# Kernel optimization log

Hardware: AMD Instinct MI355X
Metric: run time of the kernel (lower is better)

The kernel has to match this reference:

```python
import jax, jax.numpy as jnp
import numpy as np

B, NPG, EPG = 8, 12500, 200000
N, E = B * NPG, B * EPG
NUM_CLASSES = 10
EPS = 1e-5
G1, G2 = 8, 4            # voxel grids: size 1/8 then 1/4 over unit square
C1 = B * G1 * G1         # coarse node count after pool5
DIMS = [(1, 16), (16, 64), (64, 64), (64, 64), (64, 128), (128, 128), (128, 128)]


def _bn_elu(x, g, b):
    # training-mode BatchNorm1d (biased var) + ELU
    m = jnp.mean(x, axis=0)
    v = jnp.var(x, axis=0)
    return jax.nn.elu(g * (x - m) * jax.lax.rsqrt(v + EPS) + b)


def _pnconv(x, pos, src, dst, wl, wg, n):
    # PointNetConv: gather endpoints, local_nn on [x_j, pos_j - pos_i], scatter-max, global_nn
    h = jnp.concatenate([x[src], pos[src] - pos[dst]], axis=-1) @ wl
    agg = jax.ops.segment_max(h, dst, num_segments=n)
    agg = jnp.where(jnp.isfinite(agg), agg, 0.0)
    return agg @ wg


def _voxel_cluster(pos2d, batch, g, cells):
    cx = jnp.clip(jnp.floor(pos2d[:, 0] * g), 0, g - 1).astype(jnp.int32)
    cy = jnp.clip(jnp.floor(pos2d[:, 1] * g), 0, g - 1).astype(jnp.int32)
    return batch.astype(jnp.int32) * cells + cx * g + cy


def _forward(x, pos, src, dst, batch, params):
    (wl1, wg1, g1, b1, wl2, wg2, g2, b2, wl3, wg3, g3, b3,
     wl4, wg4, g4, b4, wl5, wg5, g5, b5, wl6, wg6, g6, b6,
     wl7, wg7, g7, b7, wfc) = params
    h = _bn_elu(_pnconv(x, pos, src, dst, wl1, wg1, N), g1, b1)
    h = _bn_elu(_pnconv(h, pos, src, dst, wl2, wg2, N), g2, b2)
    sc = h
    h = _bn_elu(_pnconv(h, pos, src, dst, wl3, wg3, N), g3, b3)
    h = _bn_elu(_pnconv(h, pos, src, dst, wl4, wg4, N), g4, b4)
    h = h + sc
    h = _bn_elu(_pnconv(h, pos, src, dst, wl5, wg5, N), g5, b5)
    # pool5: voxel max-pool of x, mean-pool of pos, coarsen edges
    clus = _voxel_cluster(pos[:, :2], batch, G1, G1 * G1)
    hc = jax.ops.segment_max(h, clus, num_segments=C1)
    hc = jnp.where(jnp.isfinite(hc), hc, 0.0)
    cnt = jax.ops.segment_sum(jnp.ones((N,), h.dtype), clus, num_segments=C1)
    posc = jax.ops.segment_sum(pos, clus, num_segments=C1) / jnp.maximum(cnt, 1.0)[:, None]
    loops = jnp.arange(C1)
    src2 = jnp.concatenate([clus[src], loops])
    dst2 = jnp.concatenate([clus[dst], loops])
    batchc = jnp.repeat(jnp.arange(B), G1 * G1)
    sc2 = hc
    h2 = _bn_elu(_pnconv(hc, posc, src2, dst2, wl6, wg6, C1), g6, b6)
    h2 = _bn_elu(_pnconv(h2, posc, src2, dst2, wl7, wg7, C1), g7, b7)
    h2 = h2 + sc2
    # pool7: 4x4 voxel max-pool -> fixed 16 cells per graph
    clus2 = _voxel_cluster(posc[:, :2], batchc, G2, G2 * G2)
    xo = jax.ops.segment_max(h2, clus2, num_segments=B * 16)
    xo = jnp.where(jnp.isfinite(xo), xo, 0.0)
    return xo.reshape(B, 16 * 128) @ wfc


def setup_inputs() -> dict:
    key = jax.random.key(0)
    ks = jax.random.split(key, 24)
    x = jax.random.normal(ks[0], (N, 1), jnp.float32)
    pos = jax.random.uniform(ks[1], (N, 3), jnp.float32)
    off = (jnp.arange(B) * NPG)[:, None]
    src = (jax.random.randint(ks[2], (B, EPG), 0, NPG) + off).reshape(-1)
    dst = (jax.random.randint(ks[3], (B, EPG), 0, NPG) + off).reshape(-1)
    loops = jnp.arange(N)
    src = jnp.concatenate([src, loops])
    dst = jnp.concatenate([dst, loops])
    batch = jnp.repeat(jnp.arange(B), NPG)
    inp = dict(x=x, pos=pos, src=src, dst=dst, batch=batch)
    ki = 4
    for i, (cin, cout) in enumerate(DIMS, 1):
        inp[f"wl{i}"] = jax.random.normal(ks[ki], (cin + 3, cout), jnp.float32) * (1.0 / np.sqrt(cin + 3))
        ki += 1
        inp[f"wg{i}"] = jax.random.normal(ks[ki], (cout, cout), jnp.float32) * (1.0 / np.sqrt(cout))
        ki += 1
        inp[f"g{i}"] = jnp.ones((cout,), jnp.float32)
        inp[f"b{i}"] = jnp.zeros((cout,), jnp.float32)
    inp["wfc"] = jax.random.normal(ks[ki], (128 * 16, NUM_CLASSES), jnp.float32) * (1.0 / np.sqrt(2048.0))
    return inp


def reference(x, pos, src, dst, batch,
              wl1, wg1, g1, b1, wl2, wg2, g2, b2, wl3, wg3, g3, b3,
              wl4, wg4, g4, b4, wl5, wg5, g5, b5, wl6, wg6, g6, b6,
              wl7, wg7, g7, b7, wfc):
    params = (wl1, wg1, g1, b1, wl2, wg2, g2, b2, wl3, wg3, g3, b3,
              wl4, wg4, g4, b4, wl5, wg5, g5, b5, wl6, wg6, g6, b6,
              wl7, wg7, g7, b7, wfc)
    return _forward(x, pos, src, dst, batch, params)
```

## Files before the change

kernel.cpp:

```cpp
#include <hip/hip_runtime.h>
#include <math.h>

#define N_NODES 100000
#define NPG     12500
#define EPG     200000
#define EPG_TOT 212500
#define E_TOT   1700000
#define C1      512
#define NB_SCAN 98
#define NSTRIPE 64
#define NCHUNK  8
#define CHUNK   26563

static inline int cdiv(int a, int b){ return (a + b - 1) / b; }

__device__ __forceinline__ unsigned fenc(float f){
  unsigned u = __float_as_uint(f);
  return (u >> 31) ? ~u : (u | 0x80000000u);
}
__device__ __forceinline__ float fdec(unsigned e){
  return (e & 0x80000000u) ? __uint_as_float(e ^ 0x80000000u) : __uint_as_float(~e);
}

__device__ __forceinline__ float elu1(float v){ return v > 0.f ? v : expm1f(v); }

__global__ void zero_kernel(int* __restrict__ p, int n){
  int i = blockIdx.x * 256 + threadIdx.x;
  if (i < n) p[i] = 0;
}

__global__ __launch_bounds__(1024) void count_deg(
    const int* __restrict__ dst, int* __restrict__ deg,
    unsigned short* __restrict__ ernk){
  __shared__ int ldeg[NPG];
  __shared__ int lbase[NPG];
  int g = blockIdx.x & 7;
  int chunk = blockIdx.x >> 3;
  int t = threadIdx.x;
  for (int j = t; j < NPG; j += 1024) ldeg[j] = 0;
  __syncthreads();
  int i0 = chunk * CHUNK;
  int i1 = min(i0 + CHUNK, EPG_TOT);
  for (int idx = i0 + t; idx < i1; idx += 1024){
    int dl = (idx < EPG) ? (dst[g * EPG + idx] - g * NPG) : (idx - EPG);
    int p = atomicAdd(&ldeg[dl], 1);
    ernk[(size_t)g * EPG_TOT + idx] = (unsigned short)p;
  }
  __syncthreads();
  for (int j = t; j < NPG; j += 1024){
    int cnt = ldeg[j];
    lbase[j] = cnt ? atomicAdd(&deg[g * NPG + j], cnt) : 0;
  }
  __syncthreads();
  for (int idx = i0 + t; idx < i1; idx += 1024){
    int dl = (idx < EPG) ? (dst[g * EPG + idx] - g * NPG) : (idx - EPG);
    ernk[(size_t)g * EPG_TOT + idx] += (unsigned short)lbase[dl];
  }
}

__global__ void scan1(const int* __restrict__ deg, int* __restrict__ row_start,
                      int* __restrict__ partials){
  __shared__ int sm[256];
  int t = threadIdx.x, b = blockIdx.x;
  int base = b * 1024 + t * 4;
  int d0 = (base + 0 < N_NODES) ? deg[base + 0] : 0;
  int d1 = (base + 1 < N_NODES) ? deg[base + 1] : 0;
  int d2 = (base + 2 < N_NODES) ? deg[base + 2] : 0;
  int d3 = (base + 3 < N_NODES) ? deg[base + 3] : 0;
  int s = d0 + d1 + d2 + d3;
  sm[t] = s; __syncthreads();
  for (int off = 1; off < 256; off <<= 1){
    int v = (t >= off) ? sm[t - off] : 0;
    __syncthreads();
    sm[t] += v;
    __syncthreads();
  }
  int excl = sm[t] - s;
  if (base + 0 < N_NODES) row_start[base + 0] = excl;
  if (base + 1 < N_NODES) row_start[base + 1] = excl + d0;
  if (base + 2 < N_NODES) row_start[base + 2] = excl + d0 + d1;
  if (base + 3 < N_NODES) row_start[base + 3] = excl + d0 + d1 + d2;
  if (t == 255) partials[b] = sm[255];
}

__global__ void scan2(int* __restrict__ partials){
  if (threadIdx.x == 0 && blockIdx.x == 0){
    int acc = 0;
    for (int i = 0; i < NB_SCAN; i++){ int v = partials[i]; partials[i] = acc; acc += v; }
  }
}

__global__ void scan3(int* __restrict__ row_start, const int* __restrict__ partials){
  int i = blockIdx.x * 256 + threadIdx.x;
  if (i < N_NODES) row_start[i] += partials[i >> 10];
  if (i == 0) row_start[N_NODES] = E_TOT;
}

__global__ void fill_csr(const int* __restrict__ src, const int* __restrict__ dst,
                         const int* __restrict__ clus, const unsigned short* __restrict__ ernk,
                         const int* __restrict__ row_start,
                         unsigned short* __restrict__ col, int* __restrict__ pf){
  int g = blockIdx.x & 7;
  int idx = (blockIdx.x >> 3) * 256 + threadIdx.x;
  if (idx >= EPG_TOT) return;
  int s, d;
  if (idx < EPG){ int e = g * EPG + idx; s = src[e]; d = dst[e]; }
  else { s = d = g * NPG + idx - EPG; }
  int p = ernk[(size_t)g * EPG_TOT + idx];
  col[row_start[d] + p] = (unsigned short)(s - g * NPG);
  pf[clus[d] * 64 + (clus[s] & 63)] = 1;
}

template<int R, int CIN, int COUT, bool FIX, bool STATS, bool BNIN, bool POSW, bool GSWZ>
__global__ __launch_bounds__(256) void gemm_tile(
    const float* __restrict__ in, const float* __restrict__ w,
    const float* __restrict__ ss, const float* __restrict__ resid,
    float* __restrict__ side, const float* __restrict__ posn,
    const float* __restrict__ w3p, float* __restrict__ out,
    float* __restrict__ stat, int n){
  constexpr int CPL = (COUT + 63) / 64;
  __shared__ float lds[4][R * CIN];
  __shared__ float sred[STATS ? 8 * COUT : 1];
  int wave = threadIdx.x >> 6, lane = threadIdx.x & 63;
  int base, nlim;
  if (GSWZ){
    int g = blockIdx.x & 7;
    base = g * NPG + ((blockIdx.x >> 3) * 4 + wave) * R;
    nlim = g * NPG + NPG;
  } else {
    base = (blockIdx.x * 4 + wave) * R;
    nlim = n;
  }

  if (base < nlim){
    const float4* src4 = (const float4*)(in + (size_t)base * CIN);
    const float4* res4 = resid ? (const float4*)(resid + (size_t)base * CIN) : nullptr;
    float4* side4 = side ? (float4*)(side + (size_t)base * CIN) : nullptr;
    float4* dst4 = (float4*)lds[wave];
    int n4 = min(R, nlim - base) * CIN / 4;
    for (int i = lane; i < R * CIN / 4; i += 64){
      float4 v = (i < n4) ? src4[i] : make_float4(0.f, 0.f, 0.f, 0.f);
      if (FIX){
        v.x = isfinite(v.x) ? v.x : 0.f; v.y = isfinite(v.y) ? v.y : 0.f;
        v.z = isfinite(v.z) ? v.z : 0.f; v.w = isfinite(v.w) ? v.w : 0.f;
      }
      if (BNIN){
        int c0 = (i * 4) & (CIN - 1);
        v.x = elu1(fmaf(v.x, ss[c0 + 0], ss[128 + c0 + 0]));
        v.y = elu1(fmaf(v.y, ss[c0 + 1], ss[128 + c0 + 1]));
        v.z = elu1(fmaf(v.z, ss[c0 + 2], ss[128 + c0 + 2]));
        v.w = elu1(fmaf(v.w, ss[c0 + 3], ss[128 + c0 + 3]));
        if (res4 && i < n4){
          float4 r = res4[i];
          v.x += r.x; v.y += r.y; v.z += r.z; v.w += r.w;
        }
        if (side4 && i < n4) side4[i] = v;
      }
      dst4[i] = v;
    }
  }
  __builtin_amdgcn_wave_barrier();

  bool act = (COUT >= 64) || (lane < COUT);
  float acc[CPL][R];
  #pragma unroll
  for (int j = 0; j < CPL; j++)
    #pragma unroll
    for (int r = 0; r < R; r++) acc[j][r] = 0.f;

  if (base < nlim && act){
    const float4* l4 = (const float4*)lds[wave];
    for (int k = 0; k < CIN; k += 4){
      float4 wv[CPL];
      #pragma unroll
      for (int j = 0; j < CPL; j++){
        int c = lane + 64 * j;
        wv[j].x = w[(k + 0) * COUT + c];
        wv[j].y = w[(k + 1) * COUT + c];
        wv[j].z = w[(k + 2) * COUT + c];
        wv[j].w = w[(k + 3) * COUT + c];
      }
      #pragma unroll
      for (int r = 0; r < R; r++){
        float4 a = l4[(r * CIN + k) >> 2];
        #pragma unroll
        for (int j = 0; j < CPL; j++)
          acc[j][r] = fmaf(a.x, wv[j].x, fmaf(a.y, wv[j].y,
                      fmaf(a.z, wv[j].z, fmaf(a.w, wv[j].w, acc[j][r]))));
      }
    }
    float q0[POSW ? CPL : 1], q1[POSW ? CPL : 1], q2[POSW ? CPL : 1];
    if (POSW){
      #pragma unroll
      for (int j = 0; j < CPL; j++){
        int c = lane + 64 * j;
        q0[j] = w3p[c]; q1[j] = w3p[COUT + c]; q2[j] = w3p[2 * COUT + c];
      }
    }
    int nrows = min(R, nlim - base);
    for (int r = 0; r < nrows; r++){
      if (POSW){
        float px = posn[(size_t)(base + r) * 3 + 0];
        float py = posn[(size_t)(base + r) * 3 + 1];
        float pz = posn[(size_t)(base + r) * 3 + 2];
        #pragma unroll
        for (int j = 0; j < CPL; j++)
          acc[j][r] = fmaf(px, q0[j], fmaf(py, q1[j], fmaf(pz, q2[j], acc[j][r])));
      }
      #pragma unroll
      for (int j = 0; j < CPL; j++)
        out[(size_t)(base + r) * COUT + lane + 64 * j] = acc[j][r];
    }
  }

  if (STATS){
    #pragma unroll
    for (int j = 0; j < CPL; j++){
      float s = 0.f, q = 0.f;
      #pragma unroll
      for (int r = 0; r < R; r++){ s += acc[j][r]; q += acc[j][r] * acc[j][r]; }
      if (act){
        int c = lane + 64 * j;
        sred[(2 * wave + 0) * COUT + c] = s;
        sred[(2 * wave + 1) * COUT + c] = q;
      }
    }
    __syncthreads();
    int c = threadIdx.x;
    if (c < COUT){
      float S = 0.f, Q = 0.f;
      #pragma unroll
      for (int wv = 0; wv < 4; wv++){
        S += sred[(2 * wv + 0) * COUT + c];
        Q += sred[(2 * wv + 1) * COUT + c];
      }
      float* st = stat + (size_t)(blockIdx.x & (NSTRIPE - 1)) * 256;
      atomicAdd(&st[c], S);
      atomicAdd(&st[128 + c], Q);
    }
  }
}

__global__ void node1_kernel(const float* __restrict__ x, const float* __restrict__ pos,
                             const float* __restrict__ wl, float* __restrict__ u){
  int i = blockIdx.x * 256 + threadIdx.x;
  if (i >= N_NODES * 16) return;
  int node = i >> 4, c = i & 15;
  float px = pos[node * 3 + 0], py = pos[node * 3 + 1], pz = pos[node * 3 + 2];
  u[i] = fmaf(x[node], wl[c],
         fmaf(px, wl[16 + c], fmaf(py, wl[32 + c], pz * wl[48 + c])));
}

template<int CPL>
__global__ __launch_bounds__(256) void edge_aggN(
    const float* __restrict__ u, int ushift,
    const unsigned short* __restrict__ col,
    const float* __restrict__ w3, int cout,
    const int* __restrict__ row_start, const float* __restrict__ pos,
    float* __restrict__ agg){
  int wave = threadIdx.x >> 6, lane = threadIdx.x & 63;
  int g = blockIdx.x & 7;
  int d = g * NPG + (blockIdx.x >> 3) * 4 + wave;
  const float* uu = u + ((size_t)(g * NPG) << ushift) + lane;
  int e0 = row_start[d], e1 = row_start[d + 1];
  float a0[CPL], a1[CPL], a2[CPL], a3[CPL];
  #pragma unroll
  for (int p = 0; p < CPL; p++){ a0[p] = a1[p] = a2[p] = a3[p] = -INFINITY; }
  for (int eb = e0; eb < e1; eb += 64){
    int m = min(64, e1 - eb);
    int sv = ((int)col[eb + min(lane, m - 1)]) << ushift;
    for (int j = 0; j < m; j += 4){
      int j1 = min(j + 1, m - 1), j2 = min(j + 2, m - 1), j3 = min(j + 3, m - 1);
      int s0 = __builtin_amdgcn_readlane(sv, j);
      int s1 = __builtin_amdgcn_readlane(sv, j1);
      int s2 = __builtin_amdgcn_readlane(sv, j2);
      int s3 = __builtin_amdgcn_readlane(sv, j3);
      #pragma unroll
      for (int p = 0; p < CPL; p++){
        a0[p] = fmaxf(a0[p], uu[s0 + 64 * p]);
        a1[p] = fmaxf(a1[p], uu[s1 + 64 * p]);
        a2[p] = fmaxf(a2[p], uu[s2 + 64 * p]);
        a3[p] = fmaxf(a3[p], uu[s3 + 64 * p]);
      }
    }
  }
  float px = pos[d * 3 + 0], py = pos[d * 3 + 1], pz = pos[d * 3 + 2];
  #pragma unroll
  for (int p = 0; p < CPL; p++){
    int c = lane + 64 * p;
    float w0 = w3[c], w1 = w3[cout + c], w2 = w3[2 * cout + c];
    float corr = fmaf(px, w0, fmaf(py, w1, pz * w2));
    agg[(size_t)d * cout + c] = fmaxf(fmaxf(a0[p], a1[p]), fmaxf(a2[p], a3[p])) - corr;
  }
}

__global__ __launch_bounds__(256) void edge_agg16(
    const float* __restrict__ u,
    const unsigned short* __restrict__ col,
    const float* __restrict__ w3,
    const int* __restrict__ row_start, const float* __restrict__ pos,
    float* __restrict__ agg){
  int wave = threadIdx.x >> 6, lane = threadIdx.x & 63;
  int slot = lane >> 4, c = lane & 15;
  int g = blockIdx.x & 7;
  int dloc = (blockIdx.x >> 3) * 16 + wave * 4 + slot;
  int d = g * NPG + dloc;
  bool vd = dloc < NPG;
  int e0 = vd ? row_start[d] : 0;
  int e1 = vd ? row_start[d + 1] : 0;
  int len = e1 - e0;
  int maxlen = max(len, __shfl_xor(len, 16, 64));
  maxlen = max(maxlen, __shfl_xor(maxlen, 32, 64));
  int cap = max(len - 1, 0);
  const float* uu = u + ((size_t)(g * NPG) << 4) + c;
  float acc0 = -INFINITY, acc1 = -INFINITY;
  for (int k = 0; k < maxlen; k += 2){
    int s0 = ((int)col[e0 + min(k, cap)]) << 4;
    int s1 = ((int)col[e0 + min(k + 1, cap)]) << 4;
    float h0 = uu[s0];
    float h1 = uu[s1];
    acc0 = (k < len) ? fmaxf(acc0, h0) : acc0;
    acc1 = (k + 1 < len) ? fmaxf(acc1, h1) : acc1;
  }
  if (vd){
    float w0 = w3[c], w1 = w3[16 + c], w2 = w3[32 + c];
    float px = pos[d * 3 + 0], py = pos[d * 3 + 1], pz = pos[d * 3 + 2];
    float corr = fmaf(px, w0, fmaf(py, w1, pz * w2));
    agg[d * 16 + c] = fmaxf(acc0, acc1) - corr;
  }
}

__global__ void bn_finalize(const float* __restrict__ stats, const float* __restrict__ g,
                            const float* __restrict__ b, int cout, float invn,
                            float* __restrict__ ss){
  int c = blockIdx.x;
  if (c >= cout) return;
  int l = threadIdx.x;
  float S = stats[l * 256 + c];
  float Q = stats[l * 256 + 128 + c];
  for (int off = 32; off > 0; off >>= 1){
    S += __shfl_down(S, off, 64);
    Q += __shfl_down(Q, off, 64);
  }
  if (l == 0){
    float mean = S * invn;
    float var = fmaxf(Q * invn - mean * mean, 0.f);
    float sc = g[c] * rsqrtf(var + 1e-5f);
    ss[c] = sc;
    ss[128 + c] = b[c] - mean * sc;
  }
}

__global__ void pool5_a(const float* __restrict__ pos, const int* __restrict__ batch,
                        int* __restrict__ clus, int* __restrict__ ccnt,
                        float* __restrict__ psum){
  int i = blockIdx.x * 256 + threadIdx.x;
  if (i >= N_NODES) return;
  int cx = min(max((int)floorf(pos[i * 3 + 0] * 8.f), 0), 7);
  int cy = min(max((int)floorf(pos[i * 3 + 1] * 8.f), 0), 7);
  int cl = batch[i] * 64 + cx * 8 + cy;
  clus[i] = cl;
  atomicAdd(&ccnt[cl], 1);
  atomicAdd(&psum[cl * 3 + 0], pos[i * 3 + 0]);
  atomicAdd(&psum[cl * 3 + 1], pos[i * 3 + 1]);
  atomicAdd(&psum[cl * 3 + 2], pos[i * 3 + 2]);
}

__global__ void cluster_scan(const int* __restrict__ ccnt, int* __restrict__ coff){
  __shared__ int sm[C1];
  int t = threadIdx.x;
  sm[t] = ccnt[t]; __syncthreads();
  for (int off = 1; off < C1; off <<= 1){
    int v = (t >= off) ? sm[t - off] : 0;
    __syncthreads();
    sm[t] += v;
    __syncthreads();
  }
  coff[t + 1] = sm[t];
  if (t == 0) coff[0] = 0;
}

__global__ void cluster_fill(const int* __restrict__ clus, const int* __restrict__ coff,
                             int* __restrict__ ccur, int* __restrict__ nb){
  int i = blockIdx.x * 256 + threadIdx.x;
  if (i >= N_NODES) return;
  int cl = clus[i];
  int p = atomicAdd(&ccur[cl], 1);
  nb[coff[cl] + p] = i;
}

__global__ __launch_bounds__(128) void pool5_g(
    const float* __restrict__ y, const float* __restrict__ ss,
    const int* __restrict__ coff, const int* __restrict__ nb,
    const int* __restrict__ ccnt, const float* __restrict__ psum,
    float* __restrict__ hcf, float* __restrict__ posc, int* __restrict__ pf){
  __shared__ int nid[128];
  int d = blockIdx.x, c = threadIdx.x;
  int b0 = coff[d], b1 = coff[d + 1];
  float a0 = -INFINITY, a1 = -INFINITY;
  for (int base = b0; base < b1; base += 128){
    int m = min(128, b1 - base);
    __syncthreads();
    if (c < m) nid[c] = nb[base + c];
    __syncthreads();
    int k = 0;
    for (; k + 2 <= m; k += 2){
      float v0 = y[(size_t)nid[k] * 128 + c];
      float v1 = y[(size_t)nid[k + 1] * 128 + c];
      a0 = fmaxf(a0, v0);
      a1 = fmaxf(a1, v1);
    }
    if (k < m) a0 = fmaxf(a0, y[(size_t)nid[k] * 128 + c]);
  }
  float acc = fmaxf(a0, a1);
  float out = (b1 > b0) ? elu1(fmaf(acc, ss[c], ss[128 + c])) : 0.f;
  hcf[d * 128 + c] = isfinite(out) ? out : 0.f;
  if (c < 3) posc[d * 3 + c] = psum[d * 3 + c] / fmaxf((float)ccnt[d], 1.f);
  if (c == 0) pf[d * 64 + (d & 63)] = 1;
}

__global__ __launch_bounds__(128) void coarse_conv(
    const float* __restrict__ u2, const float* __restrict__ posc,
    const float* __restrict__ wl, const int* __restrict__ pf,
    const float* __restrict__ wg, float* __restrict__ y2,
    float* __restrict__ stat){
  __shared__ float sagg[128];
  int d = blockIdx.x, c = threadIdx.x;
  int g = d >> 6;
  float acc = -INFINITY;
  for (int j = 0; j < 64; ++j){
    if (pf[d * 64 + j]){
      int s = g * 64 + j;
      acc = fmaxf(acc, u2[s * 128 + c]);
    }
  }
  const float* wb = wl + 128 * 128;
  float w0 = wb[c], w1 = wb[128 + c], w2 = wb[256 + c];
  float px = posc[d * 3 + 0], py = posc[d * 3 + 1], pz = posc[d * 3 + 2];
  float corr = fmaf(px, w0, fmaf(py, w1, pz * w2));
  acc -= corr;
  sagg[c] = isfinite(acc) ? acc : 0.f;
  __syncthreads();
  float y = 0.f;
  for (int k = 0; k < 128; ++k) y = fmaf(sagg[k], wg[k * 128 + c], y);
  y2[d * 128 + c] = y;
  float* st = stat + (size_t)(d & (NSTRIPE - 1)) * 256;
  atomicAdd(&st[c], y);
  atomicAdd(&st[128 + c], y * y);
}

__global__ void pool7(const float* __restrict__ y2, const float* __restrict__ ss,
                      const float* __restrict__ hcf, const float* __restrict__ posc,
                      unsigned* __restrict__ xoe){
  int i = blockIdx.x, c = threadIdx.x;
  int g = i >> 6;
  float v = elu1(fmaf(y2[i * 128 + c], ss[c], ss[128 + c])) + hcf[i * 128 + c];
  int cx = min(max((int)floorf(posc[i * 3 + 0] * 4.f), 0), 3);
  int cy = min(max((int)floorf(posc[i * 3 + 1] * 4.f), 0), 3);
  int cl2 = g * 16 + cx * 4 + cy;
  atomicMax(&xoe[cl2 * 128 + c], fenc(v));
}

__global__ void fc_kernel(const unsigned* __restrict__ xoe, const float* __restrict__ wfc,
                          float* __restrict__ out){
  int o = blockIdx.x;
  int b = o / 10, cls = o % 10;
  int lane = threadIdx.x;
  float s = 0.f;
  for (int k = lane; k < 2048; k += 64){
    float v = fdec(xoe[b * 2048 + k]);
    v = isfinite(v) ? v : 0.f;
    s = fmaf(v, wfc[k * 10 + cls], s);
  }
  for (int off = 32; off > 0; off >>= 1) s += __shfl_down(s, off, 64);
  if (lane == 0) out[o] = s;
}

extern "C" void kernel_launch(void* const* d_in, const int* in_sizes, int n_in,
                              void* d_out, int out_size, void* d_ws, size_t ws_size,
                              hipStream_t stream){
  (void)in_sizes; (void)n_in; (void)out_size; (void)ws_size;
  const float* X   = (const float*)d_in[0];
  const float* POS = (const float*)d_in[1];
  const int*   SRC = (const int*)d_in[2];
  const int*   DST = (const int*)d_in[3];
  const int*   BAT = (const int*)d_in[4];
  const float* WL[7]; const float* WG[7]; const float* GG[7]; const float* BB[7];
  for (int i = 0; i < 7; i++){
    WL[i] = (const float*)d_in[5 + 4 * i];
    WG[i] = (const float*)d_in[6 + 4 * i];
    GG[i] = (const float*)d_in[7 + 4 * i];
    BB[i] = (const float*)d_in[8 + 4 * i];
  }
  const float* WFC = (const float*)d_in[33];
  float* OUT = (float*)d_out;

  float* wsf = (float*)d_ws;
  size_t o = 0;
  auto alloc = [&](size_t nf){ float* p = wsf + o; o += nf; return p; };
  float* F1   = alloc((size_t)N_NODES * 64);
  float* U    = alloc((size_t)N_NODES * 128);
  float* AG   = alloc((size_t)N_NODES * 128);
  float* HCF  = alloc(C1 * 128);
  float* POSC = alloc(2048);
  float* U2   = alloc(C1 * 128);
  float* Y2   = alloc(C1 * 128);
  float* SS   = alloc(9 * 256);
  unsigned short* COL  = (unsigned short*)alloc(E_TOT / 2 + 64);
  unsigned short* ERNK = (unsigned short*)alloc(E_TOT / 2 + 64);
  int* ROWS = (int*)alloc(N_NODES + 8);
  int* PART = (int*)alloc(256);
  int* CLUS = (int*)alloc(N_NODES);
  int* NB   = (int*)alloc(N_NODES);
  int* COFF = (int*)alloc(C1 + 8);
  int* ZZ = (int*)(wsf + o);
  int*      DEG  = (int*)alloc(N_NODES);
  float*    STAT = alloc((size_t)9 * NSTRIPE * 256);
  int*      CCNT = (int*)alloc(512);
  int*      CCUR = (int*)alloc(512);
  float*    PSUM = alloc(2048);
  int*      PF   = (int*)alloc(C1 * 64);
  unsigned* XOE  = (unsigned*)alloc(128 * 128);
  int zz_n = (int)((int*)(wsf + o) - ZZ);

  zero_kernel<<<cdiv(zz_n, 256), 256, 0, stream>>>(ZZ, zz_n);

  pool5_a<<<cdiv(N_NODES, 256), 256, 0, stream>>>(POS, BAT, CLUS, CCNT, PSUM);
  cluster_scan<<<1, C1, 0, stream>>>(CCNT, COFF);
  cluster_fill<<<cdiv(N_NODES, 256), 256, 0, stream>>>(CLUS, COFF, CCUR, NB);

  count_deg<<<8 * NCHUNK, 1024, 0, stream>>>(DST, DEG, ERNK);
  scan1<<<NB_SCAN, 256, 0, stream>>>(DEG, ROWS, PART);
  scan2<<<1, 1, 0, stream>>>(PART);
  scan3<<<cdiv(N_NODES, 256), 256, 0, stream>>>(ROWS, PART);
  dim3 gF(8 * cdiv(EPG_TOT, 256));
  fill_csr<<<gF, 256, 0, stream>>>(SRC, DST, CLUS, ERNK, ROWS, COL, PF);

  dim3 gE(8 * (NPG / 4)), bE(256);
  dim3 gE16(8 * cdiv(NPG, 16));
  dim3 gT(8 * cdiv(NPG, 32)), bT(256);
  dim3 gC(cdiv(C1, 32));

  const size_t LSTAT = (size_t)NSTRIPE * 256;
  const float invN = 1.f / N_NODES;
  auto fin = [&](int li, int cout, float invn){
    bn_finalize<<<128, 64, 0, stream>>>(STAT + li * LSTAT, GG[li], BB[li], cout, invn, SS + li * 256);
  };

  node1_kernel<<<cdiv(N_NODES * 16, 256), 256, 0, stream>>>(X, POS, WL[0], U);
  edge_agg16<<<gE16, bE, 0, stream>>>(U, COL, WL[0] + 16, ROWS, POS, AG);
  gemm_tile<8, 16, 16, true, true, false, false, true><<<gT, bT, 0, stream>>>(
      AG, WG[0], nullptr, nullptr, nullptr, nullptr, nullptr, AG, STAT + 0 * LSTAT, N_NODES);
  fin(0, 16, invN);

  gemm_tile<8, 16, 64, false, false, true, true, true><<<gT, bT, 0, stream>>>(
      AG, WL[1], SS + 0 * 256, nullptr, nullptr, POS, WL[1] + 16 * 64, U, nullptr, N_NODES);
  edge_aggN<1><<<gE, bE, 0, stream>>>(U, 6, COL, WL[1] + 16 * 64, 64, ROWS, POS, AG);
  gemm_tile<8, 64, 64, true, true, false, false, true><<<gT, bT, 0, stream>>>(
      AG, WG[1], nullptr, nullptr, nullptr, nullptr, nullptr, AG, STAT + 1 * LSTAT, N_NODES);
  fin(1, 64, invN);

  gemm_tile<8, 64, 64, false, false, true, true, true><<<gT, bT, 0, stream>>>(
      AG, WL[2], SS + 1 * 256, nullptr, F1, POS, WL[2] + 64 * 64, U, nullptr, N_NODES);
  edge_aggN<1><<<gE, bE, 0, stream>>>(U, 6, COL, WL[2] + 64 * 64, 64, ROWS, POS, AG);
  gemm_tile<8, 64, 64, true, true, false, false, true><<<gT, bT, 0, stream>>>(
      AG, WG[2], nullptr, nullptr, nullptr, nullptr, nullptr, AG, STAT + 2 * LSTAT, N_NODES);
  fin(2, 64, invN);

  gemm_tile<8, 64, 64, false, false, true, true, true><<<gT, bT, 0, stream>>>(
      AG, WL[3], SS + 2 * 256, nullptr, nullptr, POS, WL[3] + 64 * 64, U, nullptr, N_NODES);
  edge_aggN<1><<<gE, bE, 0, stream>>>(U, 6, COL, WL[3] + 64 * 64, 64, ROWS, POS, AG);
  gemm_tile<8, 64, 64, true, true, false, false, true><<<gT, bT, 0, stream>>>(
      AG, WG[3], nullptr, nullptr, nullptr, nullptr, nullptr, AG, STAT + 3 * LSTAT, N_NODES);
  fin(3, 64, invN);

  gemm_tile<8, 64, 128, false, false, true, true, true><<<gT, bT, 0, stream>>>(
      AG, WL[4], SS + 3 * 256, F1, nullptr, POS, WL[4] + 64 * 128, U, nullptr, N_NODES);
  edge_aggN<2><<<gE, bE, 0, stream>>>(U, 7, COL, WL[4] + 64 * 128, 128, ROWS, POS, AG);
  gemm_tile<8, 128, 128, true, true, false, false, true><<<gT, bT, 0, stream>>>(
      AG, WG[4], nullptr, nullptr, nullptr, nullptr, nullptr, AG, STAT + 4 * LSTAT, N_NODES);
  fin(4, 128, invN);

  pool5_g<<<C1, 128, 0, stream>>>(AG, SS + 4 * 256, COFF, NB, CCNT, PSUM, HCF, POSC, PF);

  gemm_tile<8, 128, 128, false, false, false, true, false><<<gC, bT, 0, stream>>>(
      HCF, WL[5], nullptr, nullptr, nullptr, POSC, WL[5] + 128 * 128, U2, nullptr, C1);
  coarse_conv<<<C1, 128, 0, stream>>>(U2, POSC, WL[5], PF, WG[5], Y2, STAT + 5 * LSTAT);
  fin(5, 128, 1.f / C1);

  gemm_tile<8, 128, 128, false, false, true, true, false><<<gC, bT, 0, stream>>>(
      Y2, WL[6], SS + 5 * 256, nullptr, nullptr, POSC, WL[6] + 128 * 128, U2, nullptr, C1);
  coarse_conv<<<C1, 128, 0, stream>>>(U2, POSC, WL[6], PF, WG[6], Y2, STAT + 6 * LSTAT);
  fin(6, 128, 1.f / C1);

  pool7<<<C1, 128, 0, stream>>>(Y2, SS + 6 * 256, HCF, POSC, XOE);
  fc_kernel<<<80, 64, 0, stream>>>(XOE, WFC, OUT);
}
```

Before: 921.0 us.

## Fuse edge max-aggregation with global_nn GEMM and BN statistics

Replaces the separate edge_aggN gather/max kernel and the following gemm_tile global_nn GEMM with one edge_gemm kernel. Each wave aggregates 8 destination rows into LDS and then multiplies them by wg in registers, writing output and BN sum/sumsq stats directly. This removes a full write and re-read of the aggregated activations and a kernel launch per layer. The trade-off is fewer waves per row of aggregation, more LDS use, and a serial per-row gather loop inside each wave that may reduce latency hiding.

```diff
diff --git a/kernel.cpp b/kernel.cpp
--- a/kernel.cpp
+++ b/kernel.cpp
@@ -220,7 +220,7 @@
       #pragma unroll
       for (int r = 0; r < R; r++){ s += acc[j][r]; q += acc[j][r] * acc[j][r]; }
       if (act){
-        int c = lane + 64 * j;
+        int c = threadIdx.x % 64 + 64 * j;
         sred[(2 * wave + 0) * COUT + c] = s;
         sred[(2 * wave + 1) * COUT + c] = q;
       }
@@ -238,6 +238,121 @@
       atomicAdd(&st[c], S);
       atomicAdd(&st[128 + c], Q);
     }
+  }
+}
+
+template<int CPL>
+__global__ __launch_bounds__(256) void edge_gemm(
+    const float* __restrict__ u, int ushift,
+    const unsigned short* __restrict__ col,
+    const int* __restrict__ row_start, const float* __restrict__ pos,
+    const float* __restrict__ w3, const float* __restrict__ wg,
+    float* __restrict__ out, float* __restrict__ stat){
+  constexpr int COUT = 64 * CPL;
+  constexpr int R = 8;
+  __shared__ float lds[4][R * COUT];
+  __shared__ float sred[8 * COUT];
+  int wave = threadIdx.x >> 6, lane = threadIdx.x & 63;
+  int g = blockIdx.x & 7;
+  int base = g * NPG + ((blockIdx.x >> 3) * 4 + wave) * R;
+  int glim = g * NPG + NPG;
+  const float* uu = u + ((size_t)(g * NPG) << ushift) + lane;
+  float* dstl = lds[wave];
+
+  for (int r = 0; r < R; ++r){
+    int d = base + r;
+    float a0[CPL], a1[CPL], a2[CPL], a3[CPL];
+    #pragma unroll
+    for (int p = 0; p < CPL; p++){ a0[p] = a1[p] = a2[p] = a3[p] = -INFINITY; }
+    if (d < glim){
+      int e0 = row_start[d], e1 = row_start[d + 1];
+      for (int eb = e0; eb < e1; eb += 64){
+        int m = min(64, e1 - eb);
+        int sv = ((int)col[eb + min(lane, m - 1)]) << ushift;
+        for (int j = 0; j < m; j += 4){
+          int j1 = min(j + 1, m - 1), j2 = min(j + 2, m - 1), j3 = min(j + 3, m - 1);
+          int s0 = __builtin_amdgcn_readlane(sv, j);
+          int s1 = __builtin_amdgcn_readlane(sv, j1);
+          int s2 = __builtin_amdgcn_readlane(sv, j2);
+          int s3 = __builtin_amdgcn_readlane(sv, j3);
+          #pragma unroll
+          for (int p = 0; p < CPL; p++){
+            a0[p] = fmaxf(a0[p], uu[s0 + 64 * p]);
+            a1[p] = fmaxf(a1[p], uu[s1 + 64 * p]);
+            a2[p] = fmaxf(a2[p], uu[s2 + 64 * p]);
+            a3[p] = fmaxf(a3[p], uu[s3 + 64 * p]);
+          }
+        }
+      }
+      float px = pos[d * 3 + 0], py = pos[d * 3 + 1], pz = pos[d * 3 + 2];
+      #pragma unroll
+      for (int p = 0; p < CPL; p++){
+        int c = lane + 64 * p;
+        float corr = fmaf(px, w3[c], fmaf(py, w3[COUT + c], pz * w3[2 * COUT + c]));
+        float h = fmaxf(fmaxf(a0[p], a1[p]), fmaxf(a2[p], a3[p])) - corr;
+        dstl[r * COUT + c] = isfinite(h) ? h : 0.f;
+      }
+    } else {
+      #pragma unroll
+      for (int p = 0; p < CPL; p++) dstl[r * COUT + lane + 64 * p] = 0.f;
+    }
+  }
+  __builtin_amdgcn_wave_barrier();
+
+  float acc[CPL][R];
+  #pragma unroll
+  for (int j = 0; j < CPL; j++)
+    #pragma unroll
+    for (int r = 0; r < R; r++) acc[j][r] = 0.f;
+
+  const float4* l4 = (const float4*)dstl;
+  for (int k = 0; k < COUT; k += 4){
+    float4 wv[CPL];
+    #pragma unroll
+    for (int j = 0; j < CPL; j++){
+      int c = lane + 64 * j;
+      wv[j].x = wg[(k + 0) * COUT + c];
+      wv[j].y = wg[(k + 1) * COUT + c];
+      wv[j].z = wg[(k + 2) * COUT + c];
+      wv[j].w = wg[(k + 3) * COUT + c];
+    }
+    #pragma unroll
+    for (int r = 0; r < R; r++){
+      float4 a = l4[(r * COUT + k) >> 2];
+      #pragma unroll
+      for (int j = 0; j < CPL; j++)
+        acc[j][r] = fmaf(a.x, wv[j].x, fmaf(a.y, wv[j].y,
+                    fmaf(a.z, wv[j].z, fmaf(a.w, wv[j].w, acc[j][r]))));
+    }
+  }
+  int nrows = min(R, glim - base);
+  for (int r = 0; r < nrows; r++){
+    #pragma unroll
+    for (int j = 0; j < CPL; j++)
+      out[(size_t)(base + r) * COUT + lane + 64 * j] = acc[j][r];
+  }
+
+  #pragma unroll
+  for (int j = 0; j < CPL; j++){
+    float s = 0.f, q = 0.f;
+    #pragma unroll
+    for (int r = 0; r < R; r++){ s += acc[j][r]; q += acc[j][r] * acc[j][r]; }
+    int c = lane + 64 * j;
+    sred[(2 * wave + 0) * COUT + c] = s;
+    sred[(2 * wave + 1) * COUT + c] = q;
+  }
+  __syncthreads();
+  int c = threadIdx.x;
+  if (c < COUT){
+    float S = 0.f, Q = 0.f;
+    #pragma unroll
+    for (int wv = 0; wv < 4; wv++){
+      S += sred[(2 * wv + 0) * COUT + c];
+      Q += sred[(2 * wv + 1) * COUT + c];
+    }
+    float* st = stat + (size_t)(blockIdx.x & (NSTRIPE - 1)) * 256;
+    atomicAdd(&st[c], S);
+    atomicAdd(&st[128 + c], Q);
   }
 }
 
@@ -249,49 +364,6 @@
   float px = pos[node * 3 + 0], py = pos[node * 3 + 1], pz = pos[node * 3 + 2];
   u[i] = fmaf(x[node], wl[c],
          fmaf(px, wl[16 + c], fmaf(py, wl[32 + c], pz * wl[48 + c])));
-}
-
-template<int CPL>
-__global__ __launch_bounds__(256) void edge_aggN(
-    const float* __restrict__ u, int ushift,
-    const unsigned short* __restrict__ col,
-    const float* __restrict__ w3, int cout,
-    const int* __restrict__ row_start, const float* __restrict__ pos,
-    float* __restrict__ agg){
-  int wave = threadIdx.x >> 6, lane = threadIdx.x & 63;
-  int g = blockIdx.x & 7;
-  int d = g * NPG + (blockIdx.x >> 3) * 4 + wave;
-  const float* uu = u + ((size_t)(g * NPG) << ushift) + lane;
-  int e0 = row_start[d], e1 = row_start[d + 1];
-  float a0[CPL], a1[CPL], a2[CPL], a3[CPL];
-  #pragma unroll
-  for (int p = 0; p < CPL; p++){ a0[p] = a1[p] = a2[p] = a3[p] = -INFINITY; }
-  for (int eb = e0; eb < e1; eb += 64){
-    int m = min(64, e1 - eb);
-    int sv = ((int)col[eb + min(lane, m - 1)]) << ushift;
-    for (int j = 0; j < m; j += 4){
-      int j1 = min(j + 1, m - 1), j2 = min(j + 2, m - 1), j3 = min(j + 3, m - 1);
-      int s0 = __builtin_amdgcn_readlane(sv, j);
-      int s1 = __builtin_amdgcn_readlane(sv, j1);
-      int s2 = __builtin_amdgcn_readlane(sv, j2);
-      int s3 = __builtin_amdgcn_readlane(sv, j3);
-      #pragma unroll
-      for (int p = 0; p < CPL; p++){
-        a0[p] = fmaxf(a0[p], uu[s0 + 64 * p]);
-        a1[p] = fmaxf(a1[p], uu[s1 + 64 * p]);
-        a2[p] = fmaxf(a2[p], uu[s2 + 64 * p]);
-        a3[p] = fmaxf(a3[p], uu[s3 + 64 * p]);
-      }
-    }
-  }
-  float px = pos[d * 3 + 0], py = pos[d * 3 + 1], pz = pos[d * 3 + 2];
-  #pragma unroll
-  for (int p = 0; p < CPL; p++){
-    int c = lane + 64 * p;
-    float w0 = w3[c], w1 = w3[cout + c], w2 = w3[2 * cout + c];
-    float corr = fmaf(px, w0, fmaf(py, w1, pz * w2));
-    agg[(size_t)d * cout + c] = fmaxf(fmaxf(a0[p], a1[p]), fmaxf(a2[p], a3[p])) - corr;
-  }
 }
 
 __global__ __launch_bounds__(256) void edge_agg16(
@@ -536,7 +608,6 @@
   dim3 gF(8 * cdiv(EPG_TOT, 256));
   fill_csr<<<gF, 256, 0, stream>>>(SRC, DST, CLUS, ERNK, ROWS, COL, PF);
 
-  dim3 gE(8 * (NPG / 4)), bE(256);
   dim3 gE16(8 * cdiv(NPG, 16));
   dim3 gT(8 * cdiv(NPG, 32)), bT(256);
   dim3 gC(cdiv(C1, 32));
@@ -548,37 +619,29 @@
   };
 
   node1_kernel<<<cdiv(N_NODES * 16, 256), 256, 0, stream>>>(X, POS, WL[0], U);
-  edge_agg16<<<gE16, bE, 0, stream>>>(U, COL, WL[0] + 16, ROWS, POS, AG);
+  edge_agg16<<<gE16, bT, 0, stream>>>(U, COL, WL[0] + 16, ROWS, POS, AG);
   gemm_tile<8, 16, 16, true, true, false, false, true><<<gT, bT, 0, stream>>>(
       AG, WG[0], nullptr, nullptr, nullptr, nullptr, nullptr, AG, STAT + 0 * LSTAT, N_NODES);
   fin(0, 16, invN);
 
   gemm_tile<8, 16, 64, false, false, true, true, true><<<gT, bT, 0, stream>>>(
       AG, WL[1], SS + 0 * 256, nullptr, nullptr, POS, WL[1] + 16 * 64, U, nullptr, N_NODES);
-  edge_aggN<1><<<gE, bE, 0, stream>>>(U, 6, COL, WL[1] + 16 * 64, 64, ROWS, POS, AG);
-  gemm_tile<8, 64, 64, true, true, false, false, true><<<gT, bT, 0, stream>>>(
-      AG, WG[1], nullptr, nullptr, nullptr, nullptr, nullptr, AG, STAT + 1 * LSTAT, N_NODES);
+  edge_gemm<1><<<gT, bT, 0, stream>>>(U, 6, COL, ROWS, POS, WL[1] + 16 * 64, WG[1], AG, STAT + 1 * LSTAT);
   fin(1, 64, invN);
 
   gemm_tile<8, 64, 64, false, false, true, true, true><<<gT, bT, 0, stream>>>(
       AG, WL[2], SS + 1 * 256, nullptr, F1, POS, WL[2] + 64 * 64, U, nullptr, N_NODES);
-  edge_aggN<1><<<gE, bE, 0, stream>>>(U, 6, COL, WL[2] + 64 * 64, 64, ROWS, POS, AG);
-  gemm_tile<8, 64, 64, true, true, false, false, true><<<gT, bT, 0, stream>>>(
-      AG, WG[2], nullptr, nullptr, nullptr, nullptr, nullptr, AG, STAT + 2 * LSTAT, N_NODES);
+  edge_gemm<1><<<gT, bT, 0, stream>>>(U, 6, COL, ROWS, POS, WL[2] + 64 * 64, WG[2], AG, STAT + 2 * LSTAT);
   fin(2, 64, invN);
 
   gemm_tile<8, 64, 64, false, false, true, true, true><<<gT, bT, 0, stream>>>(
       AG, WL[3], SS + 2 * 256, nullptr, nullptr, POS, WL[3] + 64 * 64, U, nullptr, N_NODES);
-  edge_aggN<1><<<gE, bE, 0, stream>>>(U, 6, COL, WL[3] + 64 * 64, 64, ROWS, POS, AG);
-  gemm_tile<8, 64, 64, true, true, false, false, true><<<gT, bT, 0, stream>>>(
-      AG, WG[3], nullptr, nullptr, nullptr, nullptr, nullptr, AG, STAT + 3 * LSTAT, N_NODES);
+  edge_gemm<1><<<gT, bT, 0, stream>>>(U, 6, COL, ROWS, POS, WL[3] + 64 * 64, WG[3], AG, STAT + 3 * LSTAT);
   fin(3, 64, invN);
 
   gemm_tile<8, 64, 128, false, false, true, true, true><<<gT, bT, 0, stream>>>(
       AG, WL[4], SS + 3 * 256, F1, nullptr, POS, WL[4] + 64 * 128, U, nullptr, N_NODES);
-  edge_aggN<2><<<gE, bE, 0, stream>>>(U, 7, COL, WL[4] + 64 * 128, 128, ROWS, POS, AG);
-  gemm_tile<8, 128, 128, true, true, false, false, true><<<gT, bT, 0, stream>>>(
-      AG, WG[4], nullptr, nullptr, nullptr, nullptr, nullptr, AG, STAT + 4 * LSTAT, N_NODES);
+  edge_gemm<2><<<gT, bT, 0, stream>>>(U, 7, COL, ROWS, POS, WL[4] + 64 * 128, WG[4], AG, STAT + 4 * LSTAT);
   fin(4, 128, invN);
 
   pool5_g<<<C1, 128, 0, stream>>>(AG, SS + 4 * 256, COFF, NB, CCNT, PSUM, HCF, POSC, PF);
```

After: 963.9 us. 1.05x slower.
